# Kernel tuning notes

Measured on AMD Instinct MI355X. Metric: run time of the kernel, lower is better.

## Reference

```python
import jax, jax.numpy as jnp
import numpy as np
from functools import partial

L, B, D_IN, D_MODEL, D_OUT, D_STATE = 2048, 8, 128, 256, 32, 16
D_INNER, DT_RANK, K_CONV = 2 * D_MODEL, D_MODEL // 16, 4
LOG2PI = float(np.log(2.0 * np.pi))


def setup_inputs() -> dict:
    key = jax.random.key(0)
    ks = jax.random.split(key, 16)
    sc = 0.02
    inp = {
        "s": jax.random.normal(ks[0], (L, B, D_IN), jnp.float32),
        "a": jax.random.normal(ks[1], (L, B, D_OUT), jnp.float32),
        # embedding linear
        "W_emb": jax.random.normal(ks[2], (D_IN, D_MODEL), jnp.float32) * sc,
        "b_emb": jnp.zeros((D_MODEL,), jnp.float32),
        # mamba block params
        "norm_w": jnp.ones((D_MODEL,), jnp.float32),
        "W_in": jax.random.normal(ks[3], (D_MODEL, 2 * D_INNER), jnp.float32) * sc,
        "conv_w": jax.random.normal(ks[4], (D_INNER, 1, K_CONV), jnp.float32) * sc,
        "conv_b": jnp.zeros((D_INNER,), jnp.float32),
        "W_x": jax.random.normal(ks[5], (D_INNER, DT_RANK + 2 * D_STATE), jnp.float32) * sc,
        "W_dt": jax.random.normal(ks[6], (DT_RANK, D_INNER), jnp.float32) * sc,
        "b_dt": jnp.full((D_INNER,), -2.0, jnp.float32),  # softplus(-2) ~ small init dt
        "A_log": jnp.broadcast_to(jnp.log(jnp.arange(1, D_STATE + 1, dtype=jnp.float32)), (D_INNER, D_STATE)).copy(),
        "D": jnp.ones((D_INNER,), jnp.float32),
        "W_out": jax.random.normal(ks[7], (D_INNER, D_MODEL), jnp.float32) * sc,
        # action head + log_std
        "W_head": jax.random.normal(ks[8], (D_MODEL, D_OUT), jnp.float32) * sc,
        "b_head": jnp.zeros((D_OUT,), jnp.float32),
        "log_std": jnp.zeros((D_OUT,), jnp.float32),
    }
    return inp


def _rmsnorm(x, w, eps=1e-5):
    return x * jax.lax.rsqrt(jnp.mean(x * x, axis=-1, keepdims=True) + eps) * w


def _silu(x):
    return x * jax.nn.sigmoid(x)


def _mamba_block(x, norm_w, W_in, conv_w, conv_b, W_x, W_dt, b_dt, A_log, D, W_out):
    # x: (B, L, d_model)
    resid = x
    xn = _rmsnorm(x, norm_w)
    xz = xn @ W_in                                  # (B, L, 2*d_inner)
    xp, z = jnp.split(xz, 2, axis=-1)
    # causal depthwise conv over time
    xc = jax.lax.conv_general_dilated(
        xp.transpose(0, 2, 1), conv_w, window_strides=(1,),
        padding=[(K_CONV - 1, 0)], feature_group_count=D_INNER,
        dimension_numbers=("NCH", "OIH", "NCH"))
    xp = _silu((xc + conv_b[None, :, None]).transpose(0, 2, 1))  # (B, L, d_inner)
    # input-dependent SSM params
    x_dbl = xp @ W_x                                # (B, L, dt_rank + 2*d_state)
    dt, Bm, Cm = jnp.split(x_dbl, [DT_RANK, DT_RANK + D_STATE], axis=-1)
    dt = jax.nn.softplus(dt @ W_dt + b_dt)          # (B, L, d_inner)
    A = -jnp.exp(A_log)                             # (d_inner, d_state)

    def step(h, t):
        dt_t, B_t, C_t, x_t = t                     # (B,d_i) (B,d_s) (B,d_s) (B,d_i)
        dA = jnp.exp(dt_t[..., None] * A)           # (B, d_inner, d_state)
        dBx = (dt_t * x_t)[..., None] * B_t[:, None, :]
        h = dA * h + dBx
        y = jnp.einsum("bds,bs->bd", h, C_t)
        return h, y

    h0 = jnp.zeros((x.shape[0], D_INNER, D_STATE), x.dtype)
    tm = lambda u: jnp.moveaxis(u, 1, 0)            # time-major
    _, ys = jax.lax.scan(step, h0, (tm(dt), tm(Bm), tm(Cm), tm(xp)))
    y = jnp.moveaxis(ys, 0, 1) + xp * D             # (B, L, d_inner)
    y = y * _silu(z)
    return y @ W_out + resid


def reference(s, a, W_emb, b_emb, norm_w, W_in, conv_w, conv_b, W_x, W_dt, b_dt,
              A_log, D, W_out, W_head, b_head, log_std):
    x = s @ W_emb + b_emb                           # (L, B, d_model)
    x = x.transpose(1, 0, 2)                        # (B, L, d_model)
    x = _mamba_block(x, norm_w, W_in, conv_w, conv_b, W_x, W_dt, b_dt, A_log, D, W_out)
    x = x.transpose(1, 0, 2)                        # (L, B, d_model)
    mu = x @ W_head + b_head                        # (L, B, d_out)
    # Normal(mu, exp(log_std)).log_prob(a).sum(-1)
    z = (a - mu) * jnp.exp(-log_std)
    logp = -0.5 * z * z - log_std - 0.5 * LOG2PI
    return logp.sum(axis=-1)                        # (L, B)
```

## Files before the change

### kernel.cpp

```cpp
#include <hip/hip_runtime.h>

typedef unsigned short u16;
typedef short bf16x8 __attribute__((ext_vector_type(8)));
typedef float floatx4 __attribute__((ext_vector_type(4)));

#define LSEQ 2048
#define BB 8
#define NTOK (LSEQ*BB)
#define DMODEL 256
#define DINNER 512
#define NSEG 128
#define SEGLEN 16

__device__ __forceinline__ float siluf(float x){ return x / (1.f + __expf(-x)); }
__device__ __forceinline__ float b2f(u16 x){ return __uint_as_float(((unsigned)x) << 16); }
__device__ __forceinline__ u16 f2b(float f){
  unsigned u = __float_as_uint(f);
  unsigned r = (u + 0x7fffu + ((u >> 16) & 1u)) >> 16;
  return (u16)r;
}

__global__ __launch_bounds__(256) void prep_k(
    const float* __restrict__ Wemb, const float* __restrict__ Win,
    const float* __restrict__ Wout, const float* __restrict__ Wx,
    const float* __restrict__ Wh,
    u16* __restrict__ WTe, u16* __restrict__ WTi, u16* __restrict__ WTo,
    u16* __restrict__ WxT, u16* __restrict__ WhT)
{
  int g = blockIdx.x, tid = threadIdx.x;
  if (g < 128) {
    int idx = g*256 + tid; int n = idx >> 7, k = idx & 127;
    WTe[idx] = f2b(Wemb[(size_t)k*256 + n]);
  } else if (g < 1152) {
    int idx = (g-128)*256 + tid; int n = idx >> 8, k = idx & 255;
    WTi[idx] = f2b(Win[(size_t)k*1024 + n]);
  } else if (g < 1664) {
    int idx = (g-1152)*256 + tid; int n = idx >> 9, k = idx & 511;
    WTo[idx] = f2b(Wout[(size_t)k*256 + n]);
  } else if (g < 1760) {
    int idx = (g-1664)*256 + tid; int n = idx >> 9, k = idx & 511;
    WxT[idx] = f2b(Wx[(size_t)k*48 + n]);
  } else {
    int idx = (g-1760)*256 + tid; int j = idx >> 8, k = idx & 255;
    WhT[idx] = f2b(Wh[(size_t)k*32 + j]);
  }
}

__global__ __launch_bounds__(256) void embnorm_k(
    const float* __restrict__ s, const u16* __restrict__ WTe,
    const float* __restrict__ bemb, const float* __restrict__ nw,
    u16* __restrict__ Xb, u16* __restrict__ XNb)
{
  __shared__ u16 SH[64*264];
  __shared__ float ssq[64*4];
  __shared__ float rr[64];
  u16* As = SH;
  u16* Bs = SH + 64*40;
  const int tid = threadIdx.x;
  const int wave = tid >> 6, lane = tid & 63;
  const int quad = lane >> 4, l16 = lane & 15;
  const int m0 = blockIdx.x*64;
  const int wn = wave*64;
  const int srow = tid >> 2, sch = (tid & 3)*8;
  floatx4 acc[4][4];
  #pragma unroll
  for (int r = 0; r < 4; ++r)
    #pragma unroll
    for (int c = 0; c < 4; ++c) acc[r][c] = (floatx4){0.f,0.f,0.f,0.f};

  for (int k0 = 0; k0 < 128; k0 += 32) {
    {
      float4 v0 = *(const float4*)&s[(size_t)(m0+srow)*128 + k0 + sch];
      float4 v1 = *(const float4*)&s[(size_t)(m0+srow)*128 + k0 + sch + 4];
      __align__(16) u16 o[8];
      o[0]=f2b(v0.x); o[1]=f2b(v0.y); o[2]=f2b(v0.z); o[3]=f2b(v0.w);
      o[4]=f2b(v1.x); o[5]=f2b(v1.y); o[6]=f2b(v1.z); o[7]=f2b(v1.w);
      *(uint4*)&As[srow*40 + sch] = *(const uint4*)o;
    }
    #pragma unroll
    for (int p = 0; p < 4; ++p) {
      int row = srow + p*64;
      *(uint4*)&Bs[row*40 + sch] = *(const uint4*)&WTe[(size_t)row*128 + k0 + sch];
    }
    __syncthreads();
    bf16x8 af[4], bf[4];
    #pragma unroll
    for (int r = 0; r < 4; ++r) af[r] = *(const bf16x8*)&As[(r*16 + l16)*40 + quad*8];
    #pragma unroll
    for (int c = 0; c < 4; ++c) bf[c] = *(const bf16x8*)&Bs[(wn + c*16 + l16)*40 + quad*8];
    #pragma unroll
    for (int r = 0; r < 4; ++r)
      #pragma unroll
      for (int c = 0; c < 4; ++c)
        acc[r][c] = __builtin_amdgcn_mfma_f32_16x16x32_bf16(af[r], bf[c], acc[r][c], 0, 0, 0);
    __syncthreads();
  }
  u16* Xs = SH;
  #pragma unroll
  for (int c = 0; c < 4; ++c) {
    int n = wn + c*16 + l16;
    float bv = bemb[n];
    #pragma unroll
    for (int r = 0; r < 4; ++r)
      #pragma unroll
      for (int reg = 0; reg < 4; ++reg) {
        int ml = r*16 + quad*4 + reg;
        Xs[ml*264 + n] = f2b(acc[r][c][reg] + bv);
      }
  }
  __syncthreads();
  #pragma unroll
  for (int p = 0; p < 8; ++p) {
    int row = p*8 + (tid >> 5);
    int col = (tid & 31)*8;
    *(uint4*)&Xb[(size_t)(m0+row)*256 + col] = *(const uint4*)&Xs[row*264 + col];
  }
  const int tk = tid >> 2, q = tid & 3;
  float ss = 0.f;
  #pragma unroll
  for (int j = 0; j < 8; ++j) {
    uint4 v = *(const uint4*)&Xs[tk*264 + q*64 + j*8];
    const u16* u = (const u16*)&v;
    #pragma unroll
    for (int i = 0; i < 8; ++i) { float x = b2f(u[i]); ss += x*x; }
  }
  ssq[tk*4 + q] = ss;
  __syncthreads();
  if (q == 0)
    rr[tk] = rsqrtf((ssq[tk*4]+ssq[tk*4+1]+ssq[tk*4+2]+ssq[tk*4+3])*(1.f/DMODEL) + 1e-5f);
  __syncthreads();
  float r = rr[tk];
  #pragma unroll
  for (int j = 0; j < 8; ++j) {
    int idx = q*64 + j*8;
    uint4 v = *(const uint4*)&Xs[tk*264 + idx];
    const u16* u = (const u16*)&v;
    float4 w0 = *(const float4*)&nw[idx];
    float4 w1 = *(const float4*)&nw[idx+4];
    __align__(16) u16 o[8];
    o[0]=f2b(b2f(u[0])*r*w0.x); o[1]=f2b(b2f(u[1])*r*w0.y);
    o[2]=f2b(b2f(u[2])*r*w0.z); o[3]=f2b(b2f(u[3])*r*w0.w);
    o[4]=f2b(b2f(u[4])*r*w1.x); o[5]=f2b(b2f(u[5])*r*w1.y);
    o[6]=f2b(b2f(u[6])*r*w1.z); o[7]=f2b(b2f(u[7])*r*w1.w);
    *(uint4*)&XNb[(size_t)(m0+tk)*256 + idx] = *(const uint4*)o;
  }
}

template<int K>
__global__ __launch_bounds__(256) void gemm_mfma(
    const u16* __restrict__ Ab, const u16* __restrict__ WT,
    u16* __restrict__ Cv, int N)
{
  __shared__ u16 SH[2*128*72];
  u16* As = SH;
  u16* Bs = SH + 128*72;
  const int tid = threadIdx.x;
  const int wave = tid >> 6, lane = tid & 63;
  const int quad = lane >> 4, l16 = lane & 15;
  const int bm0 = blockIdx.x*128, bn0 = blockIdx.y*128;
  const int wm = (wave & 1)*64, wn = (wave >> 1)*64;
  const int srow = tid >> 3, sch = (tid & 7)*8;
  floatx4 acc[4][4];
  #pragma unroll
  for (int r = 0; r < 4; ++r)
    #pragma unroll
    for (int c = 0; c < 4; ++c) acc[r][c] = (floatx4){0.f,0.f,0.f,0.f};

  for (int k0 = 0; k0 < K; k0 += 64) {
    #pragma unroll
    for (int p = 0; p < 4; ++p) {
      int row = srow + p*32;
      *(uint4*)&As[row*72 + sch] = *(const uint4*)&Ab[(size_t)(bm0+row)*K + k0 + sch];
      *(uint4*)&Bs[row*72 + sch] = *(const uint4*)&WT[(size_t)(bn0+row)*K + k0 + sch];
    }
    __syncthreads();
    #pragma unroll
    for (int ks = 0; ks < 2; ++ks) {
      bf16x8 af[4], bf[4];
      #pragma unroll
      for (int r = 0; r < 4; ++r)
        af[r] = *(const bf16x8*)&As[(wm + r*16 + l16)*72 + ks*32 + quad*8];
      #pragma unroll
      for (int c = 0; c < 4; ++c)
        bf[c] = *(const bf16x8*)&Bs[(wn + c*16 + l16)*72 + ks*32 + quad*8];
      #pragma unroll
      for (int r = 0; r < 4; ++r)
        #pragma unroll
        for (int c = 0; c < 4; ++c)
          acc[r][c] = __builtin_amdgcn_mfma_f32_16x16x32_bf16(af[r], bf[c], acc[r][c], 0, 0, 0);
    }
    __syncthreads();
  }
  u16* Cs = SH;
  #pragma unroll
  for (int c = 0; c < 4; ++c) {
    int nl = wn + c*16 + l16;
    #pragma unroll
    for (int r = 0; r < 4; ++r)
      #pragma unroll
      for (int reg = 0; reg < 4; ++reg) {
        int ml = wm + r*16 + quad*4 + reg;
        Cs[ml*136 + nl] = f2b(acc[r][c][reg]);
      }
  }
  __syncthreads();
  #pragma unroll
  for (int p = 0; p < 8; ++p) {
    int row = p*16 + (tid >> 4);
    int col = (tid & 15)*8;
    uint4 v = *(const uint4*)&Cs[row*136 + col];
    *(uint4*)&Cv[(size_t)(bm0+row)*N + bn0 + col] = v;
  }
}

__global__ __launch_bounds__(256) void xdblBC_k(const u16* __restrict__ XZb,
    const float* __restrict__ cw, const float* __restrict__ cb,
    const u16* __restrict__ WxT,
    float* __restrict__ BM, float* __restrict__ CM, float* __restrict__ DTR)
{
  __shared__ u16 As[64*40];
  __shared__ u16 Ws[48*40];
  __shared__ float CWs[512*4];
  __shared__ float CBs[512];
  const int tid = threadIdx.x;
  const int wave = tid >> 6, lane = tid & 63;
  const int quad = lane >> 4, l16 = lane & 15;
  const int m0 = blockIdx.x*64;
  const int srow = tid >> 2, sch = (tid & 3)*8;
  const int n = m0 + srow;
  for (int e = tid; e < 2048; e += 256) CWs[e] = cw[e];
  for (int e = tid; e < 512;  e += 256) CBs[e] = cb[e];
  floatx4 acc[3];
  #pragma unroll
  for (int j = 0; j < 3; ++j) acc[j] = (floatx4){0.f,0.f,0.f,0.f};
  __syncthreads();
  const bf16x8 z8 = {0,0,0,0,0,0,0,0};
  for (int k0 = 0; k0 < DINNER; k0 += 32) {
    bf16x8 t3 = *(const bf16x8*)&XZb[(size_t)n*1024 + k0 + sch];
    bf16x8 t2 = z8, t1 = z8, t0v = z8;
    if (n >= 8)  t2  = *(const bf16x8*)&XZb[(size_t)(n-8)*1024  + k0 + sch];
    if (n >= 16) t1  = *(const bf16x8*)&XZb[(size_t)(n-16)*1024 + k0 + sch];
    if (n >= 24) t0v = *(const bf16x8*)&XZb[(size_t)(n-24)*1024 + k0 + sch];
    __align__(16) u16 outa[8];
    #pragma unroll
    for (int j = 0; j < 8; ++j) {
      int c = k0 + sch + j;
      float4 wv = *(const float4*)&CWs[c*4];
      float xc = CBs[c] + wv.x*b2f((u16)t0v[j]) + wv.y*b2f((u16)t1[j])
               + wv.z*b2f((u16)t2[j]) + wv.w*b2f((u16)t3[j]);
      outa[j] = f2b(siluf(xc));
    }
    *(uint4*)&As[srow*40 + sch] = *(const uint4*)outa;
    if (tid < 192) {
      int wr = tid >> 2;
      *(uint4*)&Ws[wr*40 + sch] = *(const uint4*)&WxT[(size_t)wr*512 + k0 + sch];
    }
    __syncthreads();
    bf16x8 af = *(const bf16x8*)&As[(wave*16 + l16)*40 + quad*8];
    #pragma unroll
    for (int j = 0; j < 3; ++j) {
      bf16x8 bf = *(const bf16x8*)&Ws[(j*16 + l16)*40 + quad*8];
      acc[j] = __builtin_amdgcn_mfma_f32_16x16x32_bf16(af, bf, acc[j], 0, 0, 0);
    }
    __syncthreads();
  }
  const int tok0 = m0 + wave*16;
  #pragma unroll
  for (int reg = 0; reg < 4; ++reg) {
    size_t t = (size_t)(tok0 + quad*4 + reg);
    BM[t*16 + l16]  = acc[1][reg];
    CM[t*16 + l16]  = acc[2][reg];
    DTR[t*16 + l16] = acc[0][reg];
  }
}

__global__ __launch_bounds__(256) void scanA_k(const float* __restrict__ DTR,
    const u16* __restrict__ XZb, const float* __restrict__ BM,
    const float* __restrict__ cw, const float* __restrict__ cb,
    const float* __restrict__ Wdt, const float* __restrict__ bdt,
    const float* __restrict__ Alog, u16* __restrict__ HENDb, float* __restrict__ DTS,
    unsigned* __restrict__ DXb)
{
  const int tid = threadIdx.x;
  const int seg = blockIdx.x, b = blockIdx.y, half = blockIdx.z;
  const int c = half*256 + tid;
  const int t0 = seg*SEGLEN;
  float As[16];
  #pragma unroll
  for (int s = 0; s < 16; ++s) As[s] = -__expf(Alog[c*16+s]);
  bool uni = true;
  #pragma unroll
  for (int s = 1; s < 16; ++s)
    uni = uni && (fabsf(As[s] - As[0]*(float)(s+1)) <= 1e-4f*(float)(s+1));
  float wdt[16];
  #pragma unroll
  for (int r = 0; r < 16; ++r) wdt[r] = Wdt[r*DINNER + c];
  const float bd = bdt[c];
  const float4 cwv = *(const float4*)&cw[c*4];
  const float cbv = cb[c];
  float h[16];
  #pragma unroll
  for (int s = 0; s < 16; ++s) h[s] = 0.f;
  float dts = 0.f;
  const size_t base = (size_t)t0*BB + b;
  const u16* xzp = XZb + base*1024 + c;
  float w0 = (t0 >= 3) ? b2f(xzp[-(size_t)3*BB*1024]) : 0.f;
  float w1 = (t0 >= 2) ? b2f(xzp[-(size_t)2*BB*1024]) : 0.f;
  float w2 = (t0 >= 1) ? b2f(xzp[-(size_t)1*BB*1024]) : 0.f;
  float xz = b2f(xzp[0]);
  size_t nb16 = base*16;
  float4 b0 = *(const float4*)&BM[nb16+0],  b1 = *(const float4*)&BM[nb16+4];
  float4 b2 = *(const float4*)&BM[nb16+8],  b3 = *(const float4*)&BM[nb16+12];
  float4 d0 = *(const float4*)&DTR[nb16+0], d1 = *(const float4*)&DTR[nb16+4];
  float4 d2 = *(const float4*)&DTR[nb16+8], d3 = *(const float4*)&DTR[nb16+12];
  for (int t = 0; t < SEGLEN; ++t) {
    float xzn = 0.f;
    float4 nb0, nb1, nb2, nb3, nd0, nd1, nd2, nd3;
    if (t+1 < SEGLEN) {
      xzn = b2f(xzp[(size_t)(t+1)*BB*1024]);
      size_t nn = nb16 + (size_t)(t+1)*BB*16;
      nb0 = *(const float4*)&BM[nn+0];  nb1 = *(const float4*)&BM[nn+4];
      nb2 = *(const float4*)&BM[nn+8];  nb3 = *(const float4*)&BM[nn+12];
      nd0 = *(const float4*)&DTR[nn+0]; nd1 = *(const float4*)&DTR[nn+4];
      nd2 = *(const float4*)&DTR[nn+8]; nd3 = *(const float4*)&DTR[nn+12];
    }
    float dsum = bd;
    dsum = fmaf(d0.x,wdt[0],dsum);  dsum = fmaf(d0.y,wdt[1],dsum);
    dsum = fmaf(d0.z,wdt[2],dsum);  dsum = fmaf(d0.w,wdt[3],dsum);
    dsum = fmaf(d1.x,wdt[4],dsum);  dsum = fmaf(d1.y,wdt[5],dsum);
    dsum = fmaf(d1.z,wdt[6],dsum);  dsum = fmaf(d1.w,wdt[7],dsum);
    dsum = fmaf(d2.x,wdt[8],dsum);  dsum = fmaf(d2.y,wdt[9],dsum);
    dsum = fmaf(d2.z,wdt[10],dsum); dsum = fmaf(d2.w,wdt[11],dsum);
    dsum = fmaf(d3.x,wdt[12],dsum); dsum = fmaf(d3.y,wdt[13],dsum);
    dsum = fmaf(d3.z,wdt[14],dsum); dsum = fmaf(d3.w,wdt[15],dsum);
    float dt = (dsum > 20.f) ? dsum : __logf(1.f + __expf(dsum));
    float xp = siluf(cbv + cwv.x*w0 + cwv.y*w1 + cwv.z*w2 + cwv.w*xz);
    w0 = w1; w1 = w2; w2 = xz;
    dts += dt;
    DXb[(((size_t)(t0+t)*BB + b)*DINNER + c)] = ((unsigned)f2b(xp) << 16) | f2b(dt);
    float dtx = dt * xp;
    const float bv[16] = {b0.x,b0.y,b0.z,b0.w, b1.x,b1.y,b1.z,b1.w,
                          b2.x,b2.y,b2.z,b2.w, b3.x,b3.y,b3.z,b3.w};
    float dA[16];
    if (uni) {
      float p = __expf(dt*As[0]);
      float p2 = p*p, p4 = p2*p2, p8 = p4*p4;
      dA[0]=p;      dA[1]=p2;     dA[2]=p2*p;   dA[3]=p4;
      dA[4]=p4*p;   dA[5]=p4*p2;  dA[6]=p4*p2*p;dA[7]=p8;
      dA[8]=p8*p;   dA[9]=p8*p2;  dA[10]=p8*p2*p; dA[11]=p8*p4;
      dA[12]=p8*p4*p; dA[13]=p8*p4*p2; dA[14]=p8*p4*p2*p; dA[15]=p8*p8;
    } else {
      #pragma unroll
      for (int s = 0; s < 16; ++s) dA[s] = __expf(dt*As[s]);
    }
    #pragma unroll
    for (int s = 0; s < 16; ++s)
      h[s] = fmaf(dA[s], h[s], dtx*bv[s]);
    xz = xzn;
    b0=nb0; b1=nb1; b2=nb2; b3=nb3;
    d0=nd0; d1=nd1; d2=nd2; d3=nd3;
  }
  u16* hp = &HENDb[(((size_t)seg*BB + b)*DINNER + c)*16];
  #pragma unroll
  for (int q = 0; q < 2; ++q) {
    ushort4 v0, v1;
    v0.x = f2b(h[q*8+0]); v0.y = f2b(h[q*8+1]); v0.z = f2b(h[q*8+2]); v0.w = f2b(h[q*8+3]);
    v1.x = f2b(h[q*8+4]); v1.y = f2b(h[q*8+5]); v1.z = f2b(h[q*8+6]); v1.w = f2b(h[q*8+7]);
    *(ushort4*)&hp[q*8]     = v0;
    *(ushort4*)&hp[q*8 + 4] = v1;
  }
  DTS[((size_t)seg*BB + b)*DINNER + c] = dts;
}

__global__ __launch_bounds__(256) void stitch_k(u16* __restrict__ HENDb,
    const float* __restrict__ DTS, const float* __restrict__ Alog)
{
  int g = blockIdx.x*256 + threadIdx.x;
  int b = g >> 13;
  int rem = g & 8191;
  int cidx = rem >> 4;
  float A = -__expf(Alog[rem]);
  float h0 = 0.f;
  for (int k = 0; k < NSEG; ++k) {
    size_t idx = (((size_t)k*BB + b) << 13) + rem;
    float hend = b2f(HENDb[idx]);
    HENDb[idx] = f2b(h0);
    float dts = DTS[((size_t)k*BB + b)*DINNER + cidx];
    h0 = fmaf(__expf(dts*A), h0, hend);
  }
}

__global__ __launch_bounds__(256) void scanC_k(const unsigned* __restrict__ DXb,
    const u16* __restrict__ XZb, const float* __restrict__ BM, const float* __restrict__ CM,
    const float* __restrict__ Alog, const float* __restrict__ Dp,
    const u16* __restrict__ H0b, u16* __restrict__ YGb)
{
  const int tid = threadIdx.x;
  const int seg = blockIdx.x, b = blockIdx.y, half = blockIdx.z;
  const int c = half*256 + tid;
  const int t0 = seg*SEGLEN;
  float As[16];
  #pragma unroll
  for (int s = 0; s < 16; ++s) As[s] = -__expf(Alog[c*16+s]);
  bool uni = true;
  #pragma unroll
  for (int s = 1; s < 16; ++s)
    uni = uni && (fabsf(As[s] - As[0]*(float)(s+1)) <= 1e-4f*(float)(s+1));
  float h[16];
  const u16* hp = &H0b[(((size_t)seg*BB + b)*DINNER + c)*16];
  #pragma unroll
  for (int q = 0; q < 4; ++q) {
    ushort4 hv = *(const ushort4*)&hp[q*4];
    h[q*4+0]=b2f(hv.x); h[q*4+1]=b2f(hv.y); h[q*4+2]=b2f(hv.z); h[q*4+3]=b2f(hv.w);
  }
  const float Dv = Dp[c];
  const size_t base = (size_t)t0*BB + b;
  const unsigned* dxp = DXb + base*DINNER + c;
  const u16* zp  = XZb + base*1024 + DINNER + c;
  u16*       ygp = YGb + base*DINNER + c;
  unsigned dx = dxp[0];
  float zg = b2f(zp[0]);
  size_t nb16 = base*16;
  float4 b0 = *(const float4*)&BM[nb16+0],  b1 = *(const float4*)&BM[nb16+4];
  float4 b2 = *(const float4*)&BM[nb16+8],  b3 = *(const float4*)&BM[nb16+12];
  float4 c0 = *(const float4*)&CM[nb16+0],  c1 = *(const float4*)&CM[nb16+4];
  float4 c2 = *(const float4*)&CM[nb16+8],  c3 = *(const float4*)&CM[nb16+12];
  for (int t = 0; t < SEGLEN; ++t) {
    unsigned dxn = 0; float zgn = 0.f;
    float4 nb0, nb1, nb2, nb3, nc0, nc1, nc2, nc3;
    if (t+1 < SEGLEN) {
      dxn = dxp[(size_t)(t+1)*BB*DINNER];
      zgn = b2f(zp[(size_t)(t+1)*BB*1024]);
      size_t nn = nb16 + (size_t)(t+1)*BB*16;
      nb0 = *(const float4*)&BM[nn+0]; nb1 = *(const float4*)&BM[nn+4];
      nb2 = *(const float4*)&BM[nn+8]; nb3 = *(const float4*)&BM[nn+12];
      nc0 = *(const float4*)&CM[nn+0]; nc1 = *(const float4*)&CM[nn+4];
      nc2 = *(const float4*)&CM[nn+8]; nc3 = *(const float4*)&CM[nn+12];
    }
    float dt = __uint_as_float(dx << 16);
    float xp = __uint_as_float(dx & 0xffff0000u);
    const float bvv[16] = {b0.x,b0.y,b0.z,b0.w, b1.x,b1.y,b1.z,b1.w,
                           b2.x,b2.y,b2.z,b2.w, b3.x,b3.y,b3.z,b3.w};
    const float cvv[16] = {c0.x,c0.y,c0.z,c0.w, c1.x,c1.y,c1.z,c1.w,
                           c2.x,c2.y,c2.z,c2.w, c3.x,c3.y,c3.z,c3.w};
    float dtx = dt * xp;
    float dA[16];
    if (uni) {
      float p = __expf(dt*As[0]);
      float p2 = p*p, p4 = p2*p2, p8 = p4*p4;
      dA[0]=p;      dA[1]=p2;     dA[2]=p2*p;   dA[3]=p4;
      dA[4]=p4*p;   dA[5]=p4*p2;  dA[6]=p4*p2*p;dA[7]=p8;
      dA[8]=p8*p;   dA[9]=p8*p2;  dA[10]=p8*p2*p; dA[11]=p8*p4;
      dA[12]=p8*p4*p; dA[13]=p8*p4*p2; dA[14]=p8*p4*p2*p; dA[15]=p8*p8;
    } else {
      #pragma unroll
      for (int s = 0; s < 16; ++s) dA[s] = __expf(dt*As[s]);
    }
    float y0 = 0.f, y1 = 0.f, y2 = 0.f, y3 = 0.f;
    #pragma unroll
    for (int q = 0; q < 4; ++q) {
      h[q*4+0] = fmaf(dA[q*4+0], h[q*4+0], dtx*bvv[q*4+0]);
      h[q*4+1] = fmaf(dA[q*4+1], h[q*4+1], dtx*bvv[q*4+1]);
      h[q*4+2] = fmaf(dA[q*4+2], h[q*4+2], dtx*bvv[q*4+2]);
      h[q*4+3] = fmaf(dA[q*4+3], h[q*4+3], dtx*bvv[q*4+3]);
      y0 = fmaf(h[q*4+0], cvv[q*4+0], y0);
      y1 = fmaf(h[q*4+1], cvv[q*4+1], y1);
      y2 = fmaf(h[q*4+2], cvv[q*4+2], y2);
      y3 = fmaf(h[q*4+3], cvv[q*4+3], y3);
    }
    float y = (y0+y1) + (y2+y3);
    ygp[(size_t)t*BB*DINNER] = f2b((y + xp*Dv) * siluf(zg));
    dx = dxn; zg = zgn;
    b0=nb0; b1=nb1; b2=nb2; b3=nb3;
    c0=nc0; c1=nc1; c2=nc2; c3=nc3;
  }
}

__global__ __launch_bounds__(256) void outhead_k(const u16* __restrict__ YGb,
    const u16* __restrict__ WTo, const u16* __restrict__ Xb,
    const u16* __restrict__ WhT, const float* __restrict__ bh,
    const float* __restrict__ lstd, const float* __restrict__ a,
    float* __restrict__ out)
{
  __shared__ u16 SH[(64+256)*72];
  u16* As = SH;
  u16* Bs = SH + 64*72;
  const int tid = threadIdx.x;
  const int wave = tid >> 6, lane = tid & 63;
  const int quad = lane >> 4, l16 = lane & 15;
  const int m0 = blockIdx.x*64;
  const int n0 = wave*64;
  const int srow = tid >> 3, sch = (tid & 7)*8;
  floatx4 acc[4][4];
  #pragma unroll
  for (int r = 0; r < 4; ++r)
    #pragma unroll
    for (int c = 0; c < 4; ++c) acc[r][c] = (floatx4){0.f,0.f,0.f,0.f};

  for (int k0 = 0; k0 < DINNER; k0 += 64) {
    #pragma unroll
    for (int p = 0; p < 2; ++p) {
      int row = srow + p*32;
      *(uint4*)&As[row*72 + sch] = *(const uint4*)&YGb[(size_t)(m0+row)*DINNER + k0 + sch];
    }
    #pragma unroll
    for (int p = 0; p < 8; ++p) {
      int row = srow + p*32;
      *(uint4*)&Bs[row*72 + sch] = *(const uint4*)&WTo[(size_t)row*DINNER + k0 + sch];
    }
    __syncthreads();
    #pragma unroll
    for (int ks = 0; ks < 2; ++ks) {
      bf16x8 af[4], bf[4];
      #pragma unroll
      for (int r = 0; r < 4; ++r)
        af[r] = *(const bf16x8*)&As[(r*16 + l16)*72 + ks*32 + quad*8];
      #pragma unroll
      for (int c = 0; c < 4; ++c)
        bf[c] = *(const bf16x8*)&Bs[(n0 + c*16 + l16)*72 + ks*32 + quad*8];
      #pragma unroll
      for (int r = 0; r < 4; ++r)
        #pragma unroll
        for (int c = 0; c < 4; ++c)
          acc[r][c] = __builtin_amdgcn_mfma_f32_16x16x32_bf16(af[r], bf[c], acc[r][c], 0, 0, 0);
    }
    __syncthreads();
  }
  u16* Xs = SH;
  #pragma unroll
  for (int p = 0; p < 8; ++p) {
    int row = p*8 + (tid >> 5);
    int col = (tid & 31)*8;
    *(uint4*)&Xs[row*264 + col] = *(const uint4*)&Xb[(size_t)(m0+row)*256 + col];
  }
  __syncthreads();
  #pragma unroll
  for (int c = 0; c < 4; ++c) {
    int n = n0 + c*16 + l16;
    #pragma unroll
    for (int r = 0; r < 4; ++r) {
      #pragma unroll
      for (int reg = 0; reg < 4; ++reg) {
        int ml = r*16 + quad*4 + reg;
        Xs[ml*264 + n] = f2b(acc[r][c][reg] + b2f(Xs[ml*264 + n]));
      }
    }
  }
  __syncthreads();
  floatx4 mu[2];
  mu[0] = (floatx4){0.f,0.f,0.f,0.f};
  mu[1] = (floatx4){0.f,0.f,0.f,0.f};
  #pragma unroll
  for (int k0 = 0; k0 < DMODEL; k0 += 32) {
    bf16x8 axf = *(const bf16x8*)&Xs[(wave*16 + l16)*264 + k0 + quad*8];
    #pragma unroll
    for (int nt = 0; nt < 2; ++nt) {
      bf16x8 bwf = *(const bf16x8*)(WhT + (size_t)(nt*16 + l16)*DMODEL + k0 + quad*8);
      mu[nt] = __builtin_amdgcn_mfma_f32_16x16x32_bf16(axf, bwf, mu[nt], 0, 0, 0);
    }
  }
  float ls0 = lstd[l16],      els0 = __expf(-ls0), bh0 = bh[l16];
  float ls1 = lstd[16 + l16], els1 = __expf(-ls1), bh1 = bh[16 + l16];
  #pragma unroll
  for (int reg = 0; reg < 4; ++reg) {
    int tok = m0 + wave*16 + quad*4 + reg;
    float m0v = mu[0][reg] + bh0;
    float m1v = mu[1][reg] + bh1;
    float z0 = (a[(size_t)tok*32 + l16]      - m0v) * els0;
    float z1 = (a[(size_t)tok*32 + 16 + l16] - m1v) * els1;
    float t = (-0.5f*z0*z0 - ls0) + (-0.5f*z1*z1 - ls1) - 2.f*0.91893853320467274f;
    t += __shfl_xor(t, 1);
    t += __shfl_xor(t, 2);
    t += __shfl_xor(t, 4);
    t += __shfl_xor(t, 8);
    if (l16 == 0) out[tok] = t;
  }
}

extern "C" void kernel_launch(void* const* d_in, const int* in_sizes, int n_in,
                              void* d_out, int out_size, void* d_ws, size_t ws_size,
                              hipStream_t stream)
{
  const float* s    = (const float*)d_in[0];
  const float* a    = (const float*)d_in[1];
  const float* Wemb = (const float*)d_in[2];
  const float* bemb = (const float*)d_in[3];
  const float* nw   = (const float*)d_in[4];
  const float* Win  = (const float*)d_in[5];
  const float* cw   = (const float*)d_in[6];
  const float* cb   = (const float*)d_in[7];
  const float* Wx   = (const float*)d_in[8];
  const float* Wdt  = (const float*)d_in[9];
  const float* bdt  = (const float*)d_in[10];
  const float* Alog = (const float*)d_in[11];
  const float* Dp   = (const float*)d_in[12];
  const float* Wout = (const float*)d_in[13];
  const float* Wh   = (const float*)d_in[14];
  const float* bh   = (const float*)d_in[15];
  const float* lstd = (const float*)d_in[16];

  u16*   Xb   = (u16*)d_ws;
  u16*   XZb  = Xb  + (size_t)NTOK*DMODEL;
  u16*   XNb  = XZb + (size_t)NTOK*1024;
  u16*   YGb  = XNb + (size_t)NTOK*DMODEL;
  u16*   WTe  = YGb + (size_t)NTOK*DINNER;
  u16*   WTi  = WTe + 256*128;
  u16*   WTo  = WTi + 1024*256;
  u16*   WxT  = WTo + 256*512;
  u16*   WhT  = WxT + 48*512;
  u16*   HENDb= WhT + 32*256;
  unsigned* DXb = (unsigned*)(HENDb + (size_t)NSEG*BB*DINNER*16);
  float* BM   = (float*)(DXb + (size_t)NTOK*DINNER);
  float* CM   = BM + (size_t)NTOK*16;
  float* DTR  = CM + (size_t)NTOK*16;
  float* DTS  = DTR + (size_t)NTOK*16;
  float* out  = (float*)d_out;

  prep_k        <<<1792,        256, 0, stream>>>(Wemb, Win, Wout, Wx, Wh,
                                                  WTe, WTi, WTo, WxT, WhT);
  embnorm_k     <<<256,         256, 0, stream>>>(s, WTe, bemb, nw, Xb, XNb);
  gemm_mfma<256><<<dim3(128,8), 256, 0, stream>>>(XNb, WTi, XZb, 1024);
  xdblBC_k      <<<256,         256, 0, stream>>>(XZb, cw, cb, WxT, BM, CM, DTR);
  scanA_k       <<<dim3(NSEG,BB,2), 256, 0, stream>>>(DTR, XZb, BM, cw, cb, Wdt, bdt,
                                                      Alog, HENDb, DTS, DXb);
  stitch_k      <<<256,         256, 0, stream>>>(HENDb, DTS, Alog);
  scanC_k       <<<dim3(NSEG,BB,2), 256, 0, stream>>>(DXb, XZb, BM, CM,
                                                      Alog, Dp, HENDb, YGb);
  outhead_k     <<<256,         256, 0, stream>>>(YGb, WTo, Xb, WhT, bh, lstd, a, out);
}
```

Baseline: 244.1 us.

## Fuse chunked scan passes and stitch into one cooperative kernel with grid syncs

```diff
diff --git a/kernel.cpp b/kernel.cpp
--- a/kernel.cpp
+++ b/kernel.cpp
@@ -1,4 +1,7 @@
 #include <hip/hip_runtime.h>
+#include <hip/hip_cooperative_groups.h>
+
+namespace cg = cooperative_groups;
 
 typedef unsigned short u16;
 typedef short bf16x8 __attribute__((ext_vector_type(8)));
@@ -10,7 +13,8 @@
 #define DMODEL 256
 #define DINNER 512
 #define NSEG 128
-#define SEGLEN 16
+#define NSEG2 64
+#define SEGLEN2 32
 
 __device__ __forceinline__ float siluf(float x){ return x / (1.f + __expf(-x)); }
 __device__ __forceinline__ float b2f(u16 x){ return __uint_as_float(((unsigned)x) << 16); }
@@ -18,6 +22,22 @@
   unsigned u = __float_as_uint(f);
   unsigned r = (u + 0x7fffu + ((u >> 16) & 1u)) >> 16;
   return (u16)r;
+}
+
+__device__ __forceinline__ void compute_dA(float dt, float As0, bool uni,
+    const float* __restrict__ Alog, int c, float* dA)
+{
+  if (uni) {
+    float p = __expf(dt*As0);
+    float p2 = p*p, p4 = p2*p2, p8 = p4*p4;
+    dA[0]=p;      dA[1]=p2;     dA[2]=p2*p;   dA[3]=p4;
+    dA[4]=p4*p;   dA[5]=p4*p2;  dA[6]=p4*p2*p;dA[7]=p8;
+    dA[8]=p8*p;   dA[9]=p8*p2;  dA[10]=p8*p2*p; dA[11]=p8*p4;
+    dA[12]=p8*p4*p; dA[13]=p8*p4*p2; dA[14]=p8*p4*p2*p; dA[15]=p8*p8;
+  } else {
+    #pragma unroll
+    for (int s = 0; s < 16; ++s) dA[s] = __expf(dt * (-__expf(Alog[c*16+s])));
+  }
 }
 
 __global__ __launch_bounds__(256) void prep_k(
@@ -274,205 +294,148 @@
   }
 }
 
-__global__ __launch_bounds__(256) void scanA_k(const float* __restrict__ DTR,
-    const u16* __restrict__ XZb, const float* __restrict__ BM,
+__global__ __launch_bounds__(256, 4) void scan_fused_k(
+    const float* __restrict__ DTR, const u16* __restrict__ XZb,
+    const float* __restrict__ BM, const float* __restrict__ CM,
     const float* __restrict__ cw, const float* __restrict__ cb,
     const float* __restrict__ Wdt, const float* __restrict__ bdt,
-    const float* __restrict__ Alog, u16* __restrict__ HENDb, float* __restrict__ DTS,
-    unsigned* __restrict__ DXb)
-{
+    const float* __restrict__ Alog, const float* __restrict__ Dp,
+    u16* __restrict__ HENDb, float* __restrict__ DTS, u16* __restrict__ YGb)
+{
+  __shared__ unsigned DXs[SEGLEN2*256];
+  __shared__ float ROWa[SEGLEN2*16];
+  __shared__ float ROWb[SEGLEN2*16];
   const int tid = threadIdx.x;
   const int seg = blockIdx.x, b = blockIdx.y, half = blockIdx.z;
   const int c = half*256 + tid;
-  const int t0 = seg*SEGLEN;
-  float As[16];
-  #pragma unroll
-  for (int s = 0; s < 16; ++s) As[s] = -__expf(Alog[c*16+s]);
+  const int t0 = seg*SEGLEN2;
+  const size_t tokbase = (size_t)t0*BB + b;
+
+  for (int idx = tid; idx < SEGLEN2*16; idx += 256) {
+    int t = idx >> 4, j = idx & 15;
+    size_t off = (tokbase + (size_t)t*BB)*16 + j;
+    ROWa[idx] = BM[off];
+    ROWb[idx] = DTR[off];
+  }
+
+  float As0 = -__expf(Alog[c*16]);
   bool uni = true;
   #pragma unroll
-  for (int s = 1; s < 16; ++s)
-    uni = uni && (fabsf(As[s] - As[0]*(float)(s+1)) <= 1e-4f*(float)(s+1));
+  for (int s = 1; s < 16; ++s) {
+    float Av = -__expf(Alog[c*16+s]);
+    uni = uni && (fabsf(Av - As0*(float)(s+1)) <= 1e-4f*(float)(s+1));
+  }
   float wdt[16];
   #pragma unroll
   for (int r = 0; r < 16; ++r) wdt[r] = Wdt[r*DINNER + c];
   const float bd = bdt[c];
   const float4 cwv = *(const float4*)&cw[c*4];
   const float cbv = cb[c];
+
   float h[16];
   #pragma unroll
   for (int s = 0; s < 16; ++s) h[s] = 0.f;
   float dts = 0.f;
-  const size_t base = (size_t)t0*BB + b;
-  const u16* xzp = XZb + base*1024 + c;
+  const u16* xzp = XZb + tokbase*1024 + c;
   float w0 = (t0 >= 3) ? b2f(xzp[-(size_t)3*BB*1024]) : 0.f;
   float w1 = (t0 >= 2) ? b2f(xzp[-(size_t)2*BB*1024]) : 0.f;
   float w2 = (t0 >= 1) ? b2f(xzp[-(size_t)1*BB*1024]) : 0.f;
   float xz = b2f(xzp[0]);
-  size_t nb16 = base*16;
-  float4 b0 = *(const float4*)&BM[nb16+0],  b1 = *(const float4*)&BM[nb16+4];
-  float4 b2 = *(const float4*)&BM[nb16+8],  b3 = *(const float4*)&BM[nb16+12];
-  float4 d0 = *(const float4*)&DTR[nb16+0], d1 = *(const float4*)&DTR[nb16+4];
-  float4 d2 = *(const float4*)&DTR[nb16+8], d3 = *(const float4*)&DTR[nb16+12];
-  for (int t = 0; t < SEGLEN; ++t) {
-    float xzn = 0.f;
-    float4 nb0, nb1, nb2, nb3, nd0, nd1, nd2, nd3;
-    if (t+1 < SEGLEN) {
-      xzn = b2f(xzp[(size_t)(t+1)*BB*1024]);
-      size_t nn = nb16 + (size_t)(t+1)*BB*16;
-      nb0 = *(const float4*)&BM[nn+0];  nb1 = *(const float4*)&BM[nn+4];
-      nb2 = *(const float4*)&BM[nn+8];  nb3 = *(const float4*)&BM[nn+12];
-      nd0 = *(const float4*)&DTR[nn+0]; nd1 = *(const float4*)&DTR[nn+4];
-      nd2 = *(const float4*)&DTR[nn+8]; nd3 = *(const float4*)&DTR[nn+12];
-    }
+  __syncthreads();
+
+  for (int t = 0; t < SEGLEN2; ++t) {
+    float xzn = (t+1 < SEGLEN2) ? b2f(xzp[(size_t)(t+1)*BB*1024]) : 0.f;
     float dsum = bd;
-    dsum = fmaf(d0.x,wdt[0],dsum);  dsum = fmaf(d0.y,wdt[1],dsum);
-    dsum = fmaf(d0.z,wdt[2],dsum);  dsum = fmaf(d0.w,wdt[3],dsum);
-    dsum = fmaf(d1.x,wdt[4],dsum);  dsum = fmaf(d1.y,wdt[5],dsum);
-    dsum = fmaf(d1.z,wdt[6],dsum);  dsum = fmaf(d1.w,wdt[7],dsum);
-    dsum = fmaf(d2.x,wdt[8],dsum);  dsum = fmaf(d2.y,wdt[9],dsum);
-    dsum = fmaf(d2.z,wdt[10],dsum); dsum = fmaf(d2.w,wdt[11],dsum);
-    dsum = fmaf(d3.x,wdt[12],dsum); dsum = fmaf(d3.y,wdt[13],dsum);
-    dsum = fmaf(d3.z,wdt[14],dsum); dsum = fmaf(d3.w,wdt[15],dsum);
+    #pragma unroll
+    for (int r = 0; r < 16; ++r) dsum = fmaf(ROWb[t*16+r], wdt[r], dsum);
     float dt = (dsum > 20.f) ? dsum : __logf(1.f + __expf(dsum));
     float xp = siluf(cbv + cwv.x*w0 + cwv.y*w1 + cwv.z*w2 + cwv.w*xz);
-    w0 = w1; w1 = w2; w2 = xz;
+    w0 = w1; w1 = w2; w2 = xz; xz = xzn;
     dts += dt;
-    DXb[(((size_t)(t0+t)*BB + b)*DINNER + c)] = ((unsigned)f2b(xp) << 16) | f2b(dt);
+    DXs[t*256 + tid] = ((unsigned)f2b(xp) << 16) | f2b(dt);
     float dtx = dt * xp;
-    const float bv[16] = {b0.x,b0.y,b0.z,b0.w, b1.x,b1.y,b1.z,b1.w,
-                          b2.x,b2.y,b2.z,b2.w, b3.x,b3.y,b3.z,b3.w};
     float dA[16];
-    if (uni) {
-      float p = __expf(dt*As[0]);
-      float p2 = p*p, p4 = p2*p2, p8 = p4*p4;
-      dA[0]=p;      dA[1]=p2;     dA[2]=p2*p;   dA[3]=p4;
-      dA[4]=p4*p;   dA[5]=p4*p2;  dA[6]=p4*p2*p;dA[7]=p8;
-      dA[8]=p8*p;   dA[9]=p8*p2;  dA[10]=p8*p2*p; dA[11]=p8*p4;
-      dA[12]=p8*p4*p; dA[13]=p8*p4*p2; dA[14]=p8*p4*p2*p; dA[15]=p8*p8;
-    } else {
-      #pragma unroll
-      for (int s = 0; s < 16; ++s) dA[s] = __expf(dt*As[s]);
-    }
+    compute_dA(dt, As0, uni, Alog, c, dA);
     #pragma unroll
     for (int s = 0; s < 16; ++s)
-      h[s] = fmaf(dA[s], h[s], dtx*bv[s]);
-    xz = xzn;
-    b0=nb0; b1=nb1; b2=nb2; b3=nb3;
-    d0=nd0; d1=nd1; d2=nd2; d3=nd3;
-  }
-  u16* hp = &HENDb[(((size_t)seg*BB + b)*DINNER + c)*16];
-  #pragma unroll
-  for (int q = 0; q < 2; ++q) {
-    ushort4 v0, v1;
-    v0.x = f2b(h[q*8+0]); v0.y = f2b(h[q*8+1]); v0.z = f2b(h[q*8+2]); v0.w = f2b(h[q*8+3]);
-    v1.x = f2b(h[q*8+4]); v1.y = f2b(h[q*8+5]); v1.z = f2b(h[q*8+6]); v1.w = f2b(h[q*8+7]);
-    *(ushort4*)&hp[q*8]     = v0;
-    *(ushort4*)&hp[q*8 + 4] = v1;
-  }
-  DTS[((size_t)seg*BB + b)*DINNER + c] = dts;
-}
-
-__global__ __launch_bounds__(256) void stitch_k(u16* __restrict__ HENDb,
-    const float* __restrict__ DTS, const float* __restrict__ Alog)
-{
-  int g = blockIdx.x*256 + threadIdx.x;
-  int b = g >> 13;
-  int rem = g & 8191;
-  int cidx = rem >> 4;
-  float A = -__expf(Alog[rem]);
-  float h0 = 0.f;
-  for (int k = 0; k < NSEG; ++k) {
-    size_t idx = (((size_t)k*BB + b) << 13) + rem;
-    float hend = b2f(HENDb[idx]);
-    HENDb[idx] = f2b(h0);
-    float dts = DTS[((size_t)k*BB + b)*DINNER + cidx];
-    h0 = fmaf(__expf(dts*A), h0, hend);
-  }
-}
-
-__global__ __launch_bounds__(256) void scanC_k(const unsigned* __restrict__ DXb,
-    const u16* __restrict__ XZb, const float* __restrict__ BM, const float* __restrict__ CM,
-    const float* __restrict__ Alog, const float* __restrict__ Dp,
-    const u16* __restrict__ H0b, u16* __restrict__ YGb)
-{
-  const int tid = threadIdx.x;
-  const int seg = blockIdx.x, b = blockIdx.y, half = blockIdx.z;
-  const int c = half*256 + tid;
-  const int t0 = seg*SEGLEN;
-  float As[16];
-  #pragma unroll
-  for (int s = 0; s < 16; ++s) As[s] = -__expf(Alog[c*16+s]);
-  bool uni = true;
-  #pragma unroll
-  for (int s = 1; s < 16; ++s)
-    uni = uni && (fabsf(As[s] - As[0]*(float)(s+1)) <= 1e-4f*(float)(s+1));
-  float h[16];
-  const u16* hp = &H0b[(((size_t)seg*BB + b)*DINNER + c)*16];
-  #pragma unroll
-  for (int q = 0; q < 4; ++q) {
-    ushort4 hv = *(const ushort4*)&hp[q*4];
-    h[q*4+0]=b2f(hv.x); h[q*4+1]=b2f(hv.y); h[q*4+2]=b2f(hv.z); h[q*4+3]=b2f(hv.w);
+      h[s] = fmaf(dA[s], h[s], dtx * ROWa[t*16+s]);
+  }
+  {
+    u16* hp = &HENDb[(((size_t)seg*BB + b)*DINNER + c)*16];
+    #pragma unroll
+    for (int q = 0; q < 2; ++q) {
+      ushort4 v0, v1;
+      v0.x = f2b(h[q*8+0]); v0.y = f2b(h[q*8+1]); v0.z = f2b(h[q*8+2]); v0.w = f2b(h[q*8+3]);
+      v1.x = f2b(h[q*8+4]); v1.y = f2b(h[q*8+5]); v1.z = f2b(h[q*8+6]); v1.w = f2b(h[q*8+7]);
+      *(ushort4*)&hp[q*8]     = v0;
+      *(ushort4*)&hp[q*8 + 4] = v1;
+    }
+    DTS[((size_t)seg*BB + b)*DINNER + c] = dts;
+  }
+  __threadfence();
+  cg::this_grid().sync();
+
+  {
+    int bid = blockIdx.x + 64*(blockIdx.y + 8*blockIdx.z);
+    int g = bid*256 + tid;
+    if (g < 65536) {
+      int bb  = g >> 13;
+      int rem = g & 8191;
+      int cidx = rem >> 4;
+      float A = -__expf(Alog[rem]);
+      float h0 = 0.f;
+      for (int k = 0; k < NSEG2; ++k) {
+        size_t idx = (((size_t)k*BB + bb) << 13) + rem;
+        float hend = b2f(HENDb[idx]);
+        HENDb[idx] = f2b(h0);
+        float ds = DTS[((size_t)k*BB + bb)*DINNER + cidx];
+        h0 = fmaf(__expf(ds*A), h0, hend);
+      }
+    }
+  }
+  __threadfence();
+  cg::this_grid().sync();
+
+  for (int idx = tid; idx < SEGLEN2*16; idx += 256) {
+    int t = idx >> 4, j = idx & 15;
+    ROWb[idx] = CM[(tokbase + (size_t)t*BB)*16 + j];
+  }
+  {
+    const u16* h0p = &HENDb[(((size_t)seg*BB + b)*DINNER + c)*16];
+    #pragma unroll
+    for (int q = 0; q < 4; ++q) {
+      ushort4 hv = *(const ushort4*)&h0p[q*4];
+      h[q*4+0]=b2f(hv.x); h[q*4+1]=b2f(hv.y); h[q*4+2]=b2f(hv.z); h[q*4+3]=b2f(hv.w);
+    }
   }
   const float Dv = Dp[c];
-  const size_t base = (size_t)t0*BB + b;
-  const unsigned* dxp = DXb + base*DINNER + c;
-  const u16* zp  = XZb + base*1024 + DINNER + c;
-  u16*       ygp = YGb + base*DINNER + c;
-  unsigned dx = dxp[0];
+  const u16* zp  = XZb + tokbase*1024 + DINNER + c;
+  u16*       ygp = YGb + tokbase*DINNER + c;
   float zg = b2f(zp[0]);
-  size_t nb16 = base*16;
-  float4 b0 = *(const float4*)&BM[nb16+0],  b1 = *(const float4*)&BM[nb16+4];
-  float4 b2 = *(const float4*)&BM[nb16+8],  b3 = *(const float4*)&BM[nb16+12];
-  float4 c0 = *(const float4*)&CM[nb16+0],  c1 = *(const float4*)&CM[nb16+4];
-  float4 c2 = *(const float4*)&CM[nb16+8],  c3 = *(const float4*)&CM[nb16+12];
-  for (int t = 0; t < SEGLEN; ++t) {
-    unsigned dxn = 0; float zgn = 0.f;
-    float4 nb0, nb1, nb2, nb3, nc0, nc1, nc2, nc3;
-    if (t+1 < SEGLEN) {
-      dxn = dxp[(size_t)(t+1)*BB*DINNER];
-      zgn = b2f(zp[(size_t)(t+1)*BB*1024]);
-      size_t nn = nb16 + (size_t)(t+1)*BB*16;
-      nb0 = *(const float4*)&BM[nn+0]; nb1 = *(const float4*)&BM[nn+4];
-      nb2 = *(const float4*)&BM[nn+8]; nb3 = *(const float4*)&BM[nn+12];
-      nc0 = *(const float4*)&CM[nn+0]; nc1 = *(const float4*)&CM[nn+4];
-      nc2 = *(const float4*)&CM[nn+8]; nc3 = *(const float4*)&CM[nn+12];
-    }
+  __syncthreads();
+  for (int t = 0; t < SEGLEN2; ++t) {
+    float zgn = (t+1 < SEGLEN2) ? b2f(zp[(size_t)(t+1)*BB*1024]) : 0.f;
+    unsigned dx = DXs[t*256 + tid];
     float dt = __uint_as_float(dx << 16);
     float xp = __uint_as_float(dx & 0xffff0000u);
-    const float bvv[16] = {b0.x,b0.y,b0.z,b0.w, b1.x,b1.y,b1.z,b1.w,
-                           b2.x,b2.y,b2.z,b2.w, b3.x,b3.y,b3.z,b3.w};
-    const float cvv[16] = {c0.x,c0.y,c0.z,c0.w, c1.x,c1.y,c1.z,c1.w,
-                           c2.x,c2.y,c2.z,c2.w, c3.x,c3.y,c3.z,c3.w};
     float dtx = dt * xp;
     float dA[16];
-    if (uni) {
-      float p = __expf(dt*As[0]);
-      float p2 = p*p, p4 = p2*p2, p8 = p4*p4;
-      dA[0]=p;      dA[1]=p2;     dA[2]=p2*p;   dA[3]=p4;
-      dA[4]=p4*p;   dA[5]=p4*p2;  dA[6]=p4*p2*p;dA[7]=p8;
-      dA[8]=p8*p;   dA[9]=p8*p2;  dA[10]=p8*p2*p; dA[11]=p8*p4;
-      dA[12]=p8*p4*p; dA[13]=p8*p4*p2; dA[14]=p8*p4*p2*p; dA[15]=p8*p8;
-    } else {
-      #pragma unroll
-      for (int s = 0; s < 16; ++s) dA[s] = __expf(dt*As[s]);
-    }
+    compute_dA(dt, As0, uni, Alog, c, dA);
     float y0 = 0.f, y1 = 0.f, y2 = 0.f, y3 = 0.f;
     #pragma unroll
     for (int q = 0; q < 4; ++q) {
-      h[q*4+0] = fmaf(dA[q*4+0], h[q*4+0], dtx*bvv[q*4+0]);
-      h[q*4+1] = fmaf(dA[q*4+1], h[q*4+1], dtx*bvv[q*4+1]);
-      h[q*4+2] = fmaf(dA[q*4+2], h[q*4+2], dtx*bvv[q*4+2]);
-      h[q*4+3] = fmaf(dA[q*4+3], h[q*4+3], dtx*bvv[q*4+3]);
-      y0 = fmaf(h[q*4+0], cvv[q*4+0], y0);
-      y1 = fmaf(h[q*4+1], cvv[q*4+1], y1);
-      y2 = fmaf(h[q*4+2], cvv[q*4+2], y2);
-      y3 = fmaf(h[q*4+3], cvv[q*4+3], y3);
+      h[q*4+0] = fmaf(dA[q*4+0], h[q*4+0], dtx*ROWa[t*16+q*4+0]);
+      h[q*4+1] = fmaf(dA[q*4+1], h[q*4+1], dtx*ROWa[t*16+q*4+1]);
+      h[q*4+2] = fmaf(dA[q*4+2], h[q*4+2], dtx*ROWa[t*16+q*4+2]);
+      h[q*4+3] = fmaf(dA[q*4+3], h[q*4+3], dtx*ROWa[t*16+q*4+3]);
+      y0 = fmaf(h[q*4+0], ROWb[t*16+q*4+0], y0);
+      y1 = fmaf(h[q*4+1], ROWb[t*16+q*4+1], y1);
+      y2 = fmaf(h[q*4+2], ROWb[t*16+q*4+2], y2);
+      y3 = fmaf(h[q*4+3], ROWb[t*16+q*4+3], y3);
     }
     float y = (y0+y1) + (y2+y3);
     ygp[(size_t)t*BB*DINNER] = f2b((y + xp*Dv) * siluf(zg));
-    dx = dxn; zg = zgn;
-    b0=nb0; b1=nb1; b2=nb2; b3=nb3;
-    c0=nc0; c1=nc1; c2=nc2; c3=nc3;
+    zg = zgn;
   }
 }
 
@@ -621,10 +584,18 @@
   embnorm_k     <<<256,         256, 0, stream>>>(s, WTe, bemb, nw, Xb, XNb);
   gemm_mfma<256><<<dim3(128,8), 256, 0, stream>>>(XNb, WTi, XZb, 1024);
   xdblBC_k      <<<256,         256, 0, stream>>>(XZb, cw, cb, WxT, BM, CM, DTR);
-  scanA_k       <<<dim3(NSEG,BB,2), 256, 0, stream>>>(DTR, XZb, BM, cw, cb, Wdt, bdt,
-                                                      Alog, HENDb, DTS, DXb);
-  stitch_k      <<<256,         256, 0, stream>>>(HENDb, DTS, Alog);
-  scanC_k       <<<dim3(NSEG,BB,2), 256, 0, stream>>>(DXb, XZb, BM, CM,
-                                                      Alog, Dp, HENDb, YGb);
+
+  {
+    void* sargs[13];
+    sargs[0]  = (void*)&DTR;  sargs[1]  = (void*)&XZb;  sargs[2]  = (void*)&BM;
+    sargs[3]  = (void*)&CM;   sargs[4]  = (void*)&cw;   sargs[5]  = (void*)&cb;
+    sargs[6]  = (void*)&Wdt;  sargs[7]  = (void*)&bdt;  sargs[8]  = (void*)&Alog;
+    sargs[9]  = (void*)&Dp;   sargs[10] = (void*)&HENDb; sargs[11] = (void*)&DTS;
+    sargs[12] = (void*)&YGb;
+    hipLaunchCooperativeKernel((const void*)scan_fused_k,
+                               dim3(NSEG2, BB, 2), dim3(256),
+                               sargs, 0, stream);
+  }
+
   outhead_k     <<<256,         256, 0, stream>>>(YGb, WTo, Xb, WhT, bh, lstd, a, out);
 }
```

After: 664.9 us. 2.72x slower.
